# Optimization experiments

Hardware: AMD Instinct MI355X
Metric: run time of the kernel (lower is better)

Reference implementation:

```python
import jax, jax.numpy as jnp
import numpy as np

D_MODEL = 768
D_LAT = 384
N_FREQ = D_MODEL // 2 + 1  # 385
INIT_S = 0.02


def _quat_linear(x, Ww, Wx, Wy, Wz, b):
    # Ww..Wz: [out_q, in_q]; x: [..., 4*in_q]
    d = Ww.shape[1]
    xw, xx, xy, xz = x[..., :d], x[..., d:2*d], x[..., 2*d:3*d], x[..., 3*d:]
    lin = lambda W, v: jnp.einsum('...i,oi->...o', v, W)
    ow = lin(Ww, xw) - lin(Wx, xx) - lin(Wy, xy) - lin(Wz, xz)
    ox = lin(Ww, xx) + lin(Wx, xw) + lin(Wy, xz) - lin(Wz, xy)
    oy = lin(Ww, xy) - lin(Wx, xz) + lin(Wy, xw) + lin(Wz, xx)
    oz = lin(Ww, xz) + lin(Wx, xy) - lin(Wy, xx) + lin(Wz, xw)
    return jnp.concatenate([ow, ox, oy, oz], axis=-1) + b


def _filter1d(x, kr, ki, n):
    X = jnp.fft.rfft(x, axis=-1)
    K = kr + 1j * ki
    return jnp.fft.irfft(X * K, n=n, axis=-1)


def setup_inputs() -> dict:
    key = jax.random.key(0)
    ks = jax.random.split(key, 16)
    rn = lambda k, shape: jax.random.normal(k, shape, dtype=jnp.float32)
    in_q_e, out_q_e = D_MODEL // 4, D_LAT // 4   # 192, 96
    in_q_d, out_q_d = D_LAT // 4, D_MODEL // 4   # 96, 192
    return {
        'x': rn(ks[0], (8, 4096, D_MODEL)),
        'enc_kr': rn(ks[1], (N_FREQ,)) * INIT_S,
        'enc_ki': rn(ks[2], (N_FREQ,)) * INIT_S,
        'dec_kr': rn(ks[3], (N_FREQ,)) * INIT_S,
        'dec_ki': rn(ks[4], (N_FREQ,)) * INIT_S,
        'enc_Ww': rn(ks[5], (out_q_e, in_q_e)) * 0.02,
        'enc_Wx': rn(ks[6], (out_q_e, in_q_e)) * 0.02,
        'enc_Wy': rn(ks[7], (out_q_e, in_q_e)) * 0.02,
        'enc_Wz': rn(ks[8], (out_q_e, in_q_e)) * 0.02,
        'enc_b': jnp.zeros((D_LAT,), jnp.float32),
        'dec_Ww': rn(ks[9], (out_q_d, in_q_d)) * 0.02,
        'dec_Wx': rn(ks[10], (out_q_d, in_q_d)) * 0.02,
        'dec_Wy': rn(ks[11], (out_q_d, in_q_d)) * 0.02,
        'dec_Wz': rn(ks[12], (out_q_d, in_q_d)) * 0.02,
        'dec_b': jnp.zeros((D_MODEL,), jnp.float32),
    }


def reference(x, enc_kr, enc_ki, dec_kr, dec_ki,
              enc_Ww, enc_Wx, enc_Wy, enc_Wz, enc_b,
              dec_Ww, dec_Wx, dec_Wy, dec_Wz, dec_b):
    # encode: spectral filter -> GELU (exact erf, matching nn.GELU) -> quaternion proj
    h = jax.nn.gelu(_filter1d(x, enc_kr, enc_ki, D_MODEL), approximate=False)
    z = _quat_linear(h, enc_Ww, enc_Wx, enc_Wy, enc_Wz, enc_b)
    # decode: quaternion proj -> spectral filter
    recon = _filter1d(_quat_linear(z, dec_Ww, dec_Wx, dec_Wy, dec_Wz, dec_b),
                      dec_kr, dec_ki, D_MODEL)
    loss = jnp.mean((recon - jax.lax.stop_gradient(x)) ** 2)
    return z, loss
```

## Files before the change

### kernel.cpp

```cpp
#include <hip/hip_runtime.h>
#include <hip/hip_bf16.h>
#include <math.h>

typedef unsigned short u16;
typedef __attribute__((ext_vector_type(8))) short s8v;
typedef __attribute__((ext_vector_type(4))) float f4v;

#define DM 768
#define DL 384

__device__ __forceinline__ u16 f2bf(float f) {
  union { float f; unsigned u; } v; v.f = f;
  unsigned r = v.u + 0x7fffu + ((v.u >> 16) & 1u);
  return (u16)(r >> 16);
}

__global__ void k_build_c2(const float* __restrict__ kr0, const float* __restrict__ ki0,
                           const float* __restrict__ kr1, const float* __restrict__ ki1,
                           float* __restrict__ c0, float* __restrict__ c1) {
  const float* kr = blockIdx.y ? kr1 : kr0;
  const float* ki = blockIdx.y ? ki1 : ki0;
  float* c = blockIdx.y ? c1 : c0;
  const int t = blockIdx.x;
  const int f = threadIdx.x;
  float s = 0.f;
  for (int ff = f; ff < 384; ff += 256) {
    if (ff >= 1) {
      int ph = (ff * t) % DM;
      float th = (float)ph * (6.283185307179586f / DM);
      float sn, cs; sincosf(th, &sn, &cs);
      s += 2.f * (kr[ff] * cs - ki[ff] * sn);
    }
  }
  if (f == 0) s += kr[0] + ((t & 1) ? -kr[384] : kr[384]);
  __shared__ float red[256];
  red[f] = s; __syncthreads();
  for (int k = 128; k > 0; k >>= 1) {
    if (f < k) red[f] += red[f + k];
    __syncthreads();
  }
  if (f == 0) c[t] = red[0] * (1.f / DM);
}

__global__ void k_rb2(const float* __restrict__ c, const float* __restrict__ b,
                      float* __restrict__ rb) {
  const int i = blockIdx.x;
  const int f = threadIdx.x;
  float s = 0.f;
  for (int j = f; j < DM; j += 256) {
    int ci = i - j; if (ci < 0) ci += DM;
    s += c[ci] * b[j];
  }
  __shared__ float red[256];
  red[f] = s; __syncthreads();
  for (int k = 128; k > 0; k >>= 1) {
    if (f < k) red[f] += red[f + k];
    __syncthreads();
  }
  if (f == 0) rb[i] = red[0];
}

__global__ void k_circ2(const float* __restrict__ c0, u16* __restrict__ B0,
                        const float* __restrict__ c1, u16* __restrict__ B1) {
  const float* c = blockIdx.y ? c1 : c0;
  u16* B = blockIdx.y ? B1 : B0;
  int idx = blockIdx.x * 256 + threadIdx.x;
  int i = idx / DM, j = idx % DM;
  int d = i - j; if (d < 0) d += DM;
  B[idx] = f2bf(c[d]);
}

__device__ __constant__ int   MI_[4][4] = {{0,1,2,3},{1,0,3,2},{2,3,0,1},{3,2,1,0}};
__device__ __constant__ float SG_[4][4] = {{1,-1,-1,-1},{1,1,-1,1},{1,1,1,-1},{1,-1,1,1}};

__global__ void k_wenc(const float* __restrict__ Ww, const float* __restrict__ Wx,
                       const float* __restrict__ Wy, const float* __restrict__ Wz,
                       u16* __restrict__ B) {
  int idx = blockIdx.x * 256 + threadIdx.x;
  int o = idx / DM, j = idx % DM;
  int p = o / 96, r = o % 96, q = j / 192, cc = j % 192;
  const float* Ws[4] = {Ww, Wx, Wy, Wz};
  B[idx] = f2bf(SG_[p][q] * Ws[MI_[p][q]][r * 192 + cc]);
}

__global__ void k_ddecT(const float* __restrict__ Ww, const float* __restrict__ Wx,
                        const float* __restrict__ Wy, const float* __restrict__ Wz,
                        u16* __restrict__ B) {
  int idx = blockIdx.x * 256 + threadIdx.x;
  int o = idx / DM, j = idx % DM;
  int p = j / 192, r = j % 192, q = o / 96, cc = o % 96;
  const float* Ws[4] = {Ww, Wx, Wy, Wz};
  B[idx] = f2bf(SG_[p][q] * Ws[MI_[p][q]][r * 96 + cc]);
}

__global__ void k_cvt(const float4* __restrict__ x, u16* __restrict__ xb) {
  int i = blockIdx.x * 256 + threadIdx.x;
  float4 v = x[i];
  union { u16 u[4]; unsigned long long q; } o;
  o.u[0] = f2bf(v.x); o.u[1] = f2bf(v.y); o.u[2] = f2bf(v.z); o.u[3] = f2bf(v.w);
  *(unsigned long long*)(xb + (size_t)i * 4) = o.q;
}

__device__ __forceinline__ void ld_lds16(const u16* g, u16* l) {
  __builtin_amdgcn_global_load_lds((const __attribute__((address_space(1))) void*)g,
                                   (__attribute__((address_space(3))) void*)l, 16, 0, 0);
}

template <int KT, int NT, int NBN, int EPI>
__global__ __launch_bounds__(512, 1) void gemm8(
    const u16* __restrict__ A, const u16* __restrict__ B,
    u16* __restrict__ outb, float* __restrict__ outf,
    const float* __restrict__ bias, const float* __restrict__ xref,
    float* __restrict__ partials) {
  __shared__ __align__(16) u16 SM[57344];
  const int t = threadIdx.x;
  const int lane = t & 63, wid = t >> 6;
  const int wrow = wid >> 2, wcol = wid & 3;
  int wg = blockIdx.x;
  { const int q = gridDim.x >> 3; wg = (wg & 7) * q + (wg >> 3); }
  const int bm = wg / NBN, bn = wg % NBN;
  constexpr int NKT = KT / 64;

  f4v acc[8][3];
#pragma unroll
  for (int m = 0; m < 8; ++m)
#pragma unroll
    for (int n = 0; n < 3; ++n) acc[m][n] = (f4v)0.f;

  const int srow = t >> 3;
  const int sgrp = (t & 7) ^ (srow & 7);
  const u16* gA = A + (size_t)(bm * 256 + srow) * KT + sgrp * 8;
  const u16* gB = B + (size_t)(bn * 192 + srow) * KT + sgrp * 8;
  const int sx = ((lane >> 4) ^ (lane & 7)) * 8;
  const int ar = (wrow * 128 + (lane & 15)) * 64;
  const int br = 32768 + (wcol * 48 + (lane & 15)) * 64;

  auto stgA = [&](int kt_, int half_) {
    const u16* g = gA + (size_t)(half_ * 128) * KT + kt_ * 64;
    u16* l = SM + (kt_ & 1) * 16384 + half_ * 8192 + t * 8;
    ld_lds16(g, l);
    ld_lds16(g + 64 * KT, l + 4096);
  };
  auto stgB = [&](int kt_, int c_) {
    const u16* g = gB + (size_t)(c_ * 64) * KT + kt_ * 64;
    ld_lds16(g, SM + 32768 + (kt_ & 1) * 12288 + c_ * 4096 + t * 8);
  };

  stgA(0, 0); stgA(0, 1); stgB(0, 0); stgB(0, 1); stgB(0, 2);
  stgA(1, 0); stgB(1, 0);
  asm volatile("s_waitcnt vmcnt(3)" ::: "memory");
  __builtin_amdgcn_sched_barrier(0);
  __builtin_amdgcn_s_barrier();

#pragma unroll 2
  for (int kt = 0; kt < NKT; ++kt) {
    const int ca = (kt & 1) * 16384;
    const int cbb = (kt & 1) * 12288;
    s8v a0[4][2], a1[4][2], b01[2][2], b2[2];
#pragma unroll
    for (int m = 0; m < 4; ++m) {
      a0[m][0] = *(const s8v*)(SM + ca + ar + m * 1024 + sx);
      a0[m][1] = *(const s8v*)(SM + ca + ar + m * 1024 + (sx ^ 32));
    }
#pragma unroll
    for (int n = 0; n < 2; ++n) {
      b01[n][0] = *(const s8v*)(SM + cbb + br + n * 1024 + sx);
      b01[n][1] = *(const s8v*)(SM + cbb + br + n * 1024 + (sx ^ 32));
    }
    if (kt + 1 < NKT) stgA(kt + 1, 1);
    __builtin_amdgcn_s_barrier();
    asm volatile("s_waitcnt lgkmcnt(0)" ::: "memory");
    __builtin_amdgcn_sched_barrier(0);
    __builtin_amdgcn_s_setprio(1);
#pragma unroll
    for (int m = 0; m < 4; ++m)
#pragma unroll
      for (int n = 0; n < 2; ++n) {
        acc[m][n] = __builtin_amdgcn_mfma_f32_16x16x32_bf16(a0[m][0], b01[n][0], acc[m][n], 0, 0, 0);
        acc[m][n] = __builtin_amdgcn_mfma_f32_16x16x32_bf16(a0[m][1], b01[n][1], acc[m][n], 0, 0, 0);
      }
    __builtin_amdgcn_s_setprio(0);
    __builtin_amdgcn_s_barrier();
#pragma unroll
    for (int m = 0; m < 4; ++m) {
      a1[m][0] = *(const s8v*)(SM + ca + ar + (4 + m) * 1024 + sx);
      a1[m][1] = *(const s8v*)(SM + ca + ar + (4 + m) * 1024 + (sx ^ 32));
    }
    if (kt + 1 < NKT) { stgB(kt + 1, 1); stgB(kt + 1, 2); }
    __builtin_amdgcn_s_barrier();
    asm volatile("s_waitcnt lgkmcnt(0)" ::: "memory");
    __builtin_amdgcn_sched_barrier(0);
    __builtin_amdgcn_s_setprio(1);
#pragma unroll
    for (int m = 0; m < 4; ++m)
#pragma unroll
      for (int n = 0; n < 2; ++n) {
        acc[4 + m][n] = __builtin_amdgcn_mfma_f32_16x16x32_bf16(a1[m][0], b01[n][0], acc[4 + m][n], 0, 0, 0);
        acc[4 + m][n] = __builtin_amdgcn_mfma_f32_16x16x32_bf16(a1[m][1], b01[n][1], acc[4 + m][n], 0, 0, 0);
      }
    __builtin_amdgcn_s_setprio(0);
    __builtin_amdgcn_s_barrier();
    b2[0] = *(const s8v*)(SM + cbb + br + 2048 + sx);
    b2[1] = *(const s8v*)(SM + cbb + br + 2048 + (sx ^ 32));
    if (kt + 2 < NKT) stgA(kt + 2, 0);
    __builtin_amdgcn_s_barrier();
    asm volatile("s_waitcnt lgkmcnt(0)" ::: "memory");
    __builtin_amdgcn_sched_barrier(0);
    __builtin_amdgcn_s_setprio(1);
#pragma unroll
    for (int m = 0; m < 4; ++m) {
      acc[4 + m][2] = __builtin_amdgcn_mfma_f32_16x16x32_bf16(a1[m][0], b2[0], acc[4 + m][2], 0, 0, 0);
      acc[4 + m][2] = __builtin_amdgcn_mfma_f32_16x16x32_bf16(a1[m][1], b2[1], acc[4 + m][2], 0, 0, 0);
    }
    __builtin_amdgcn_s_setprio(0);
    __builtin_amdgcn_s_barrier();
    if (kt + 2 < NKT) {
      stgB(kt + 2, 0);
      asm volatile("s_waitcnt vmcnt(3)" ::: "memory");
    } else {
      asm volatile("s_waitcnt vmcnt(0)" ::: "memory");
    }
    __builtin_amdgcn_sched_barrier(0);
    __builtin_amdgcn_s_barrier();
    __builtin_amdgcn_s_setprio(1);
#pragma unroll
    for (int m = 0; m < 4; ++m) {
      acc[m][2] = __builtin_amdgcn_mfma_f32_16x16x32_bf16(a0[m][0], b2[0], acc[m][2], 0, 0, 0);
      acc[m][2] = __builtin_amdgcn_mfma_f32_16x16x32_bf16(a0[m][1], b2[1], acc[m][2], 0, 0, 0);
    }
    __builtin_amdgcn_s_setprio(0);
    __builtin_amdgcn_s_barrier();
  }

  if constexpr (EPI == 2) {
    float bc[3];
#pragma unroll
    for (int n = 0; n < 3; ++n) bc[n] = bias[bn * 192 + wcol * 48 + n * 16 + (lane & 15)];
    float ls = 0.f;
#pragma unroll
    for (int m = 0; m < 8; ++m)
#pragma unroll
      for (int n = 0; n < 3; ++n)
#pragma unroll
        for (int j = 0; j < 4; ++j) {
          size_t row = bm * 256 + wrow * 128 + m * 16 + (lane >> 4) * 4 + j;
          int col = bn * 192 + wcol * 48 + n * 16 + (lane & 15);
          float v = acc[m][n][j] + bc[n];
          float d = v - xref[row * NT + col];
          ls += d * d;
        }
#pragma unroll
    for (int o = 32; o > 0; o >>= 1) ls += __shfl_down(ls, o);
    float* rw = (float*)SM;
    if (lane == 0) rw[wid] = ls;
    __syncthreads();
    if (t == 0) {
      float s = 0.f;
#pragma unroll
      for (int i = 0; i < 8; ++i) s += rw[i];
      partials[blockIdx.x] = s;
    }
  } else {
    float bc[3];
    if constexpr (EPI == 1) {
#pragma unroll
      for (int n = 0; n < 3; ++n) bc[n] = bias[bn * 192 + wcol * 48 + n * 16 + (lane & 15)];
    }
    for (int ch = 0; ch < 2; ++ch) {
      if (wrow == ch) {
#pragma unroll
        for (int m = 0; m < 8; ++m)
#pragma unroll
          for (int n = 0; n < 3; ++n)
#pragma unroll
            for (int j = 0; j < 4; ++j) {
              float v = acc[m][n][j];
              if constexpr (EPI == 0) {
                float u = v * 0.70710678118f, u2 = u * u;
                float p = u * (1.1283791671f + u2 * (-0.37612638903f +
                          u2 * (0.11283791671f + u2 * (-0.02686617064f))));
                v = 0.5f * v * (1.f + p);
              } else {
                v += bc[n];
                outf[(size_t)(bm * 256 + ch * 128 + m * 16 + (lane >> 4) * 4 + j) * NT
                     + bn * 192 + wcol * 48 + n * 16 + (lane & 15)] = v;
              }
              SM[(m * 16 + (lane >> 4) * 4 + j) * 200 + wcol * 48 + n * 16 + (lane & 15)] = f2bf(v);
            }
      }
      __syncthreads();
#pragma unroll
      for (int it = 0; it < 6; ++it) {
        int idx = it * 512 + t;
        int r = idx / 24, c8 = (idx % 24) * 8;
        s8v vv = *(const s8v*)(SM + r * 200 + c8);
        *(s8v*)(outb + (size_t)(bm * 256 + ch * 128 + r) * NT + bn * 192 + c8) = vv;
      }
      __syncthreads();
    }
  }
}

template <int KT, int NT, int NBN>
__global__ __launch_bounds__(256, 3) void gemm_ring(
    const u16* __restrict__ A, const u16* __restrict__ B, u16* __restrict__ outb) {
  __shared__ __align__(16) u16 SMR[24576];
#define As_(b) (SMR + (b) * 4096)
#define Bs_(b) (SMR + 12288 + (b) * 4096)
  const int t = threadIdx.x;
  const int wid = t >> 6, lane = t & 63;
  const int wr = wid >> 1, wc = wid & 1;
  const int bm = blockIdx.x / NBN, bn = blockIdx.x % NBN;

  f4v acc[4][4];
#pragma unroll
  for (int m = 0; m < 4; ++m)
#pragma unroll
    for (int n = 0; n < 4; ++n) acc[m][n] = (f4v)0.f;

  const int sgo = ((t & 3) ^ ((t >> 3) & 3)) * 8;
  const u16* gA = A + (size_t)(bm * 128 + (t >> 2)) * KT + sgo;
  const u16* gB = B + (size_t)(bn * 128 + (t >> 2)) * KT + sgo;
  const int fr = lane & 15;
  const int fo = ((lane >> 4) ^ ((fr >> 1) & 3)) * 8;
  constexpr int NK = KT / 32;

  auto stage = [&](int kt_, int b_) {
    const int ko = kt_ * 32;
    ld_lds16(gA + ko, As_(b_) + wid * 512);
    ld_lds16(gA + ko + 64 * KT, As_(b_) + wid * 512 + 2048);
    ld_lds16(gB + ko, Bs_(b_) + wid * 512);
    ld_lds16(gB + ko + 64 * KT, Bs_(b_) + wid * 512 + 2048);
  };

  stage(0, 0);
  stage(1, 1);
#pragma unroll 3
  for (int kt = 0; kt < NK; ++kt) {
    const int b0 = kt % 3, b2 = (kt + 2) % 3;
    if (kt + 2 < NK) stage(kt + 2, b2);
    const int ahead = NK - 1 - kt;
    if (ahead >= 2)      { asm volatile("s_waitcnt vmcnt(8)" ::: "memory"); }
    else if (ahead == 1) { asm volatile("s_waitcnt vmcnt(4)" ::: "memory"); }
    else                 { asm volatile("s_waitcnt vmcnt(0)" ::: "memory"); }
    __builtin_amdgcn_sched_barrier(0);
    __builtin_amdgcn_s_barrier();
    s8v af[4], bfv[4];
#pragma unroll
    for (int m = 0; m < 4; ++m)
      af[m] = *(const s8v*)(As_(b0) + (wr * 64 + m * 16 + fr) * 32 + fo);
#pragma unroll
    for (int n = 0; n < 4; ++n)
      bfv[n] = *(const s8v*)(Bs_(b0) + (wc * 64 + n * 16 + fr) * 32 + fo);
    asm volatile("s_waitcnt lgkmcnt(0)" ::: "memory");
    __builtin_amdgcn_sched_barrier(0);
    __builtin_amdgcn_s_barrier();
    __builtin_amdgcn_s_setprio(1);
#pragma unroll
    for (int m = 0; m < 4; ++m)
#pragma unroll
      for (int n = 0; n < 4; ++n)
        acc[m][n] = __builtin_amdgcn_mfma_f32_16x16x32_bf16(af[m], bfv[n], acc[m][n], 0, 0, 0);
    __builtin_amdgcn_s_setprio(0);
  }

  const int r0l = wr * 64 + ((lane >> 4) << 2);
  const int c0l = wc * 64 + (lane & 15);
  u16* Cs = SMR;
#pragma unroll
  for (int m = 0; m < 4; ++m)
#pragma unroll
    for (int n = 0; n < 4; ++n)
#pragma unroll
      for (int j = 0; j < 4; ++j)
        Cs[(r0l + m * 16 + j) * 130 + c0l + n * 16] = f2bf(acc[m][n][j]);
  __syncthreads();
#pragma unroll
  for (int s = 0; s < 8; ++s) {
    int idx = (s * 256 + t) * 8;
    int r = idx >> 7, c = idx & 127;
    s8v vv = *(const s8v*)(Cs + r * 130 + c);
    *(s8v*)(outb + (size_t)(bm * 128 + r) * NT + bn * 128 + c) = vv;
  }
#undef As_
#undef Bs_
}

__global__ void k_loss_final(const float* __restrict__ partials, float* __restrict__ out) {
  __shared__ float red[256];
  float s = 0.f;
  for (int i = threadIdx.x; i < 512; i += 256) s += partials[i];
  red[threadIdx.x] = s; __syncthreads();
  for (int k = 128; k > 0; k >>= 1) {
    if (threadIdx.x < k) red[threadIdx.x] += red[threadIdx.x + k];
    __syncthreads();
  }
  if (threadIdx.x == 0) out[0] = red[0] / 25165824.f;
}

extern "C" void kernel_launch(void* const* d_in, const int* in_sizes, int n_in,
                              void* d_out, int out_size, void* d_ws, size_t ws_size,
                              hipStream_t stream) {
  const float* x      = (const float*)d_in[0];
  const float* enc_kr = (const float*)d_in[1];
  const float* enc_ki = (const float*)d_in[2];
  const float* dec_kr = (const float*)d_in[3];
  const float* dec_ki = (const float*)d_in[4];
  const float* enc_Ww = (const float*)d_in[5];
  const float* enc_Wx = (const float*)d_in[6];
  const float* enc_Wy = (const float*)d_in[7];
  const float* enc_Wz = (const float*)d_in[8];
  const float* enc_b  = (const float*)d_in[9];
  const float* dec_Ww = (const float*)d_in[10];
  const float* dec_Wx = (const float*)d_in[11];
  const float* dec_Wy = (const float*)d_in[12];
  const float* dec_Wz = (const float*)d_in[13];
  const float* dec_b  = (const float*)d_in[14];

  char* ws = (char*)d_ws;
  float* c_enc    = (float*)(ws + 0);
  float* c_dec    = (float*)(ws + 4096);
  float* rb       = (float*)(ws + 8192);
  float* partials = (float*)(ws + 12288);
  u16*   Benc     = (u16*)(ws + 20480);
  u16*   Wenc     = (u16*)(ws + 1200128);
  u16*   Mdec     = (u16*)(ws + 1789952);
  u16*   Cdec     = (u16*)(ws + 2379776);
  u16*   DdT      = (u16*)(ws + 3559424);
  u16*   Xb       = (u16*)(ws + 4149248);
  u16*   Zb       = Xb;
  u16*   H        = (u16*)(ws + 54480896);

  k_build_c2<<<dim3(768, 2), 256, 0, stream>>>(enc_kr, enc_ki, dec_kr, dec_ki, c_enc, c_dec);
  k_rb2<<<768, 256, 0, stream>>>(c_dec, dec_b, rb);
  k_circ2<<<dim3(2304, 2), 256, 0, stream>>>(c_enc, Benc, c_dec, Cdec);
  k_wenc<<<1152, 256, 0, stream>>>(enc_Ww, enc_Wx, enc_Wy, enc_Wz, Wenc);
  k_ddecT<<<1152, 256, 0, stream>>>(dec_Ww, dec_Wx, dec_Wy, dec_Wz, DdT);
  gemm_ring<768, 384, 3><<<18, 256, 0, stream>>>(Cdec, DdT, Mdec);
  k_cvt<<<24576, 256, 0, stream>>>((const float4*)x, Xb);

  float* zout = (float*)d_out;
  gemm8<768, 768, 4, 0><<<512, 512, 0, stream>>>(Xb, Benc, H, nullptr, nullptr, nullptr, nullptr);
  gemm8<768, 384, 2, 1><<<256, 512, 0, stream>>>(H, Wenc, Zb, zout, enc_b, nullptr, nullptr);
  gemm8<384, 768, 4, 2><<<512, 512, 0, stream>>>(Zb, Mdec, nullptr, nullptr, rb, x, partials);
  k_loss_final<<<1, 256, 0, stream>>>(partials, zout + (out_size - 1));
}
```

Before: 186.7 us.

## Run encoder and decoder GEMMs with 128x128 ring kernel, loss against bf16 x

The second and third GEMMs move from the 256x192 single-block-per-CU kernel to the smaller 128x128 ring kernel with 3 blocks per CU. That kernel gains bias, fp32 output, swizzled block order and fused loss epilogues. The loss epilogue now reads the bf16 copy of x instead of fp32 x, halving reference traffic but adding rounding error to the loss. Z gets its own buffer instead of aliasing Xb, since Xb must stay valid for the loss.

Result: faster. 167.1 us (-10.5%).

```diff
diff --git a/kernel.cpp b/kernel.cpp
--- a/kernel.cpp
+++ b/kernel.cpp
@@ -13,6 +13,9 @@
   union { float f; unsigned u; } v; v.f = f;
   unsigned r = v.u + 0x7fffu + ((v.u >> 16) & 1u);
   return (u16)(r >> 16);
+}
+__device__ __forceinline__ float bf2f(u16 b) {
+  union { unsigned u; float f; } v; v.u = ((unsigned)b) << 16; return v.f;
 }
 
 __global__ void k_build_c2(const float* __restrict__ kr0, const float* __restrict__ ki0,
@@ -106,20 +109,16 @@
                                    (__attribute__((address_space(3))) void*)l, 16, 0, 0);
 }
 
-template <int KT, int NT, int NBN, int EPI>
-__global__ __launch_bounds__(512, 1) void gemm8(
-    const u16* __restrict__ A, const u16* __restrict__ B,
-    u16* __restrict__ outb, float* __restrict__ outf,
-    const float* __restrict__ bias, const float* __restrict__ xref,
-    float* __restrict__ partials) {
+__global__ __launch_bounds__(512, 1) void gemm8_g1(
+    const u16* __restrict__ A, const u16* __restrict__ B, u16* __restrict__ outb) {
   __shared__ __align__(16) u16 SM[57344];
   const int t = threadIdx.x;
   const int lane = t & 63, wid = t >> 6;
   const int wrow = wid >> 2, wcol = wid & 3;
   int wg = blockIdx.x;
   { const int q = gridDim.x >> 3; wg = (wg & 7) * q + (wg >> 3); }
-  const int bm = wg / NBN, bn = wg % NBN;
-  constexpr int NKT = KT / 64;
+  const int bm = wg >> 2, bn = wg & 3;
+  constexpr int KT = 768, NT = 768, NKT = KT / 64;
 
   f4v acc[8][3];
 #pragma unroll
@@ -232,85 +231,49 @@
     __builtin_amdgcn_s_barrier();
   }
 
-  if constexpr (EPI == 2) {
-    float bc[3];
-#pragma unroll
-    for (int n = 0; n < 3; ++n) bc[n] = bias[bn * 192 + wcol * 48 + n * 16 + (lane & 15)];
-    float ls = 0.f;
-#pragma unroll
-    for (int m = 0; m < 8; ++m)
-#pragma unroll
-      for (int n = 0; n < 3; ++n)
-#pragma unroll
-        for (int j = 0; j < 4; ++j) {
-          size_t row = bm * 256 + wrow * 128 + m * 16 + (lane >> 4) * 4 + j;
-          int col = bn * 192 + wcol * 48 + n * 16 + (lane & 15);
-          float v = acc[m][n][j] + bc[n];
-          float d = v - xref[row * NT + col];
-          ls += d * d;
-        }
-#pragma unroll
-    for (int o = 32; o > 0; o >>= 1) ls += __shfl_down(ls, o);
-    float* rw = (float*)SM;
-    if (lane == 0) rw[wid] = ls;
-    __syncthreads();
-    if (t == 0) {
-      float s = 0.f;
-#pragma unroll
-      for (int i = 0; i < 8; ++i) s += rw[i];
-      partials[blockIdx.x] = s;
-    }
-  } else {
-    float bc[3];
-    if constexpr (EPI == 1) {
-#pragma unroll
-      for (int n = 0; n < 3; ++n) bc[n] = bias[bn * 192 + wcol * 48 + n * 16 + (lane & 15)];
-    }
-    for (int ch = 0; ch < 2; ++ch) {
-      if (wrow == ch) {
-#pragma unroll
-        for (int m = 0; m < 8; ++m)
-#pragma unroll
-          for (int n = 0; n < 3; ++n)
-#pragma unroll
-            for (int j = 0; j < 4; ++j) {
-              float v = acc[m][n][j];
-              if constexpr (EPI == 0) {
-                float u = v * 0.70710678118f, u2 = u * u;
-                float p = u * (1.1283791671f + u2 * (-0.37612638903f +
-                          u2 * (0.11283791671f + u2 * (-0.02686617064f))));
-                v = 0.5f * v * (1.f + p);
-              } else {
-                v += bc[n];
-                outf[(size_t)(bm * 256 + ch * 128 + m * 16 + (lane >> 4) * 4 + j) * NT
-                     + bn * 192 + wcol * 48 + n * 16 + (lane & 15)] = v;
-              }
-              SM[(m * 16 + (lane >> 4) * 4 + j) * 200 + wcol * 48 + n * 16 + (lane & 15)] = f2bf(v);
-            }
-      }
-      __syncthreads();
-#pragma unroll
-      for (int it = 0; it < 6; ++it) {
-        int idx = it * 512 + t;
-        int r = idx / 24, c8 = (idx % 24) * 8;
-        s8v vv = *(const s8v*)(SM + r * 200 + c8);
-        *(s8v*)(outb + (size_t)(bm * 256 + ch * 128 + r) * NT + bn * 192 + c8) = vv;
-      }
-      __syncthreads();
-    }
-  }
-}
-
-template <int KT, int NT, int NBN>
+  for (int ch = 0; ch < 2; ++ch) {
+    if (wrow == ch) {
+#pragma unroll
+      for (int m = 0; m < 8; ++m)
+#pragma unroll
+        for (int n = 0; n < 3; ++n)
+#pragma unroll
+          for (int j = 0; j < 4; ++j) {
+            float v = acc[m][n][j];
+            float u = v * 0.70710678118f, u2 = u * u;
+            float p = u * (1.1283791671f + u2 * (-0.37612638903f +
+                      u2 * (0.11283791671f + u2 * (-0.02686617064f))));
+            v = 0.5f * v * (1.f + p);
+            SM[(m * 16 + (lane >> 4) * 4 + j) * 200 + wcol * 48 + n * 16 + (lane & 15)] = f2bf(v);
+          }
+    }
+    __syncthreads();
+#pragma unroll
+    for (int it = 0; it < 6; ++it) {
+      int idx = it * 512 + t;
+      int r = idx / 24, c8 = (idx % 24) * 8;
+      s8v vv = *(const s8v*)(SM + r * 200 + c8);
+      *(s8v*)(outb + (size_t)(bm * 256 + ch * 128 + r) * NT + bn * 192 + c8) = vv;
+    }
+    __syncthreads();
+  }
+}
+
+template <int KT, int NT, int NBN, int EPI, int SWZ>
 __global__ __launch_bounds__(256, 3) void gemm_ring(
-    const u16* __restrict__ A, const u16* __restrict__ B, u16* __restrict__ outb) {
+    const u16* __restrict__ A, const u16* __restrict__ B,
+    u16* __restrict__ outb, float* __restrict__ outf,
+    const float* __restrict__ bias, const u16* __restrict__ xref,
+    float* __restrict__ partials) {
   __shared__ __align__(16) u16 SMR[24576];
 #define As_(b) (SMR + (b) * 4096)
 #define Bs_(b) (SMR + 12288 + (b) * 4096)
   const int t = threadIdx.x;
   const int wid = t >> 6, lane = t & 63;
   const int wr = wid >> 1, wc = wid & 1;
-  const int bm = blockIdx.x / NBN, bn = blockIdx.x % NBN;
+  int wg = blockIdx.x;
+  if (SWZ) { const int q = gridDim.x >> 3; wg = (wg & 7) * q + (wg >> 3); }
+  const int bm = wg / NBN, bn = wg % NBN;
 
   f4v acc[4][4];
 #pragma unroll
@@ -366,21 +329,58 @@
 
   const int r0l = wr * 64 + ((lane >> 4) << 2);
   const int c0l = wc * 64 + (lane & 15);
-  u16* Cs = SMR;
-#pragma unroll
-  for (int m = 0; m < 4; ++m)
-#pragma unroll
-    for (int n = 0; n < 4; ++n)
-#pragma unroll
-      for (int j = 0; j < 4; ++j)
-        Cs[(r0l + m * 16 + j) * 130 + c0l + n * 16] = f2bf(acc[m][n][j]);
-  __syncthreads();
-#pragma unroll
-  for (int s = 0; s < 8; ++s) {
-    int idx = (s * 256 + t) * 8;
-    int r = idx >> 7, c = idx & 127;
-    s8v vv = *(const s8v*)(Cs + r * 130 + c);
-    *(s8v*)(outb + (size_t)(bm * 128 + r) * NT + bn * 128 + c) = vv;
+
+  if constexpr (EPI == 2) {
+    float bc[4];
+#pragma unroll
+    for (int n = 0; n < 4; ++n) bc[n] = bias[bn * 128 + c0l + n * 16];
+    float ls = 0.f;
+#pragma unroll
+    for (int m = 0; m < 4; ++m)
+#pragma unroll
+      for (int n = 0; n < 4; ++n)
+#pragma unroll
+        for (int j = 0; j < 4; ++j) {
+          size_t row = bm * 128 + r0l + m * 16 + j;
+          int col = bn * 128 + c0l + n * 16;
+          float v = acc[m][n][j] + bc[n];
+          float d = v - bf2f(xref[row * NT + col]);
+          ls += d * d;
+        }
+#pragma unroll
+    for (int o = 32; o > 0; o >>= 1) ls += __shfl_down(ls, o);
+    float* rw = (float*)SMR;
+    if (lane == 0) rw[wid] = ls;
+    __syncthreads();
+    if (t == 0) partials[blockIdx.x] = rw[0] + rw[1] + rw[2] + rw[3];
+  } else {
+    u16* Cs = SMR;
+    float bc[4];
+    if constexpr (EPI == 1) {
+#pragma unroll
+      for (int n = 0; n < 4; ++n) bc[n] = bias[bn * 128 + c0l + n * 16];
+    }
+#pragma unroll
+    for (int m = 0; m < 4; ++m)
+#pragma unroll
+      for (int n = 0; n < 4; ++n)
+#pragma unroll
+        for (int j = 0; j < 4; ++j) {
+          float v = acc[m][n][j];
+          if constexpr (EPI == 1) {
+            v += bc[n];
+            outf[(size_t)(bm * 128 + r0l + m * 16 + j) * NT + bn * 128 + c0l + n * 16] = v;
+          }
+          Cs[(r0l + m * 16 + j) * 130 + c0l + n * 16] = f2bf(v);
+        }
+    __syncthreads();
+#pragma unroll
+    for (int s = 0; s < 8; ++s) {
+      int idx = (s * 256 + t) * 8;
+      int r = idx >> 7, c = idx & 127;
+      s8v vv = *(const s8v*)(Cs + r * 130 + c);
+      *(s8v*)(outb + (size_t)(bm * 128 + r) * NT + bn * 128 + c) = vv;
+    }
   }
 #undef As_
 #undef Bs_
@@ -389,7 +389,7 @@
 __global__ void k_loss_final(const float* __restrict__ partials, float* __restrict__ out) {
   __shared__ float red[256];
   float s = 0.f;
-  for (int i = threadIdx.x; i < 512; i += 256) s += partials[i];
+  for (int i = threadIdx.x; i < 1536; i += 256) s += partials[i];
   red[threadIdx.x] = s; __syncthreads();
   for (int k = 128; k > 0; k >>= 1) {
     if (threadIdx.x < k) red[threadIdx.x] += red[threadIdx.x + k];
@@ -428,20 +428,20 @@
   u16*   Cdec     = (u16*)(ws + 2379776);
   u16*   DdT      = (u16*)(ws + 3559424);
   u16*   Xb       = (u16*)(ws + 4149248);
-  u16*   Zb       = Xb;
   u16*   H        = (u16*)(ws + 54480896);
+  u16*   Zb       = (u16*)(ws + 104812544);
 
   k_build_c2<<<dim3(768, 2), 256, 0, stream>>>(enc_kr, enc_ki, dec_kr, dec_ki, c_enc, c_dec);
   k_rb2<<<768, 256, 0, stream>>>(c_dec, dec_b, rb);
   k_circ2<<<dim3(2304, 2), 256, 0, stream>>>(c_enc, Benc, c_dec, Cdec);
   k_wenc<<<1152, 256, 0, stream>>>(enc_Ww, enc_Wx, enc_Wy, enc_Wz, Wenc);
   k_ddecT<<<1152, 256, 0, stream>>>(dec_Ww, dec_Wx, dec_Wy, dec_Wz, DdT);
-  gemm_ring<768, 384, 3><<<18, 256, 0, stream>>>(Cdec, DdT, Mdec);
+  gemm_ring<768, 384, 3, 3, 0><<<18, 256, 0, stream>>>(Cdec, DdT, Mdec, nullptr, nullptr, nullptr, nullptr);
   k_cvt<<<24576, 256, 0, stream>>>((const float4*)x, Xb);
 
   float* zout = (float*)d_out;
-  gemm8<768, 768, 4, 0><<<512, 512, 0, stream>>>(Xb, Benc, H, nullptr, nullptr, nullptr, nullptr);
-  gemm8<768, 384, 2, 1><<<256, 512, 0, stream>>>(H, Wenc, Zb, zout, enc_b, nullptr, nullptr);
-  gemm8<384, 768, 4, 2><<<512, 512, 0, stream>>>(Zb, Mdec, nullptr, nullptr, rb, x, partials);
+  gemm8_g1<<<512, 512, 0, stream>>>(Xb, Benc, H);
+  gemm_ring<768, 384, 3, 1, 1><<<768, 256, 0, stream>>>(H, Wenc, Zb, zout, enc_b, nullptr, nullptr);
+  gemm_ring<384, 768, 6, 2, 1><<<1536, 256, 0, stream>>>(Zb, Mdec, nullptr, nullptr, rb, Xb, partials);
   k_loss_final<<<1, 256, 0, stream>>>(partials, zout + (out_size - 1));
 }
```
